# Kernel tuning notes

Hardware: AMD Instinct MI355X
Metric: run time of the kernel (lower is better)

## Reference

```python
import jax, jax.numpy as jnp
import numpy as np

B, L = 8, 2048
AMP, ANG = 48, 16
H = 4
AQK, GQK = 12, 6   # amp/ang qk head dims
AV, GV = 12, 6     # amp/ang v head dims
LOOKBACK = 100


def setup_inputs() -> dict:
    key = jax.random.key(0)
    ks = jax.random.split(key, 16)
    def w(k, i, o):
        # kaiming-uniform-ish scale; stored [in, out] so forward is x @ W
        bound = 1.0 / np.sqrt(i)
        return jax.random.uniform(k, (i, o), jnp.float32, -bound, bound)
    return dict(
        x_ang=jax.random.normal(ks[0], (B, L, 2 * ANG), jnp.float32),
        x_amp=jax.random.normal(ks[1], (B, L, AMP), jnp.float32),
        Wq_amp=w(ks[2], AMP, H * AQK),
        Wk_amp=w(ks[3], AMP, H * AQK),
        Wv_amp=w(ks[4], AMP, H * AV),
        Wq_ang_r=w(ks[5], ANG, H * GQK),
        Wq_ang_i=w(ks[6], ANG, H * GQK),
        Wk_ang_r=w(ks[7], ANG, H * GQK),
        Wk_ang_i=w(ks[8], ANG, H * GQK),
        Wv_ang_r=w(ks[9], ANG, H * GV),
        Wv_ang_i=w(ks[10], ANG, H * GV),
        Wout_amp=w(ks[11], H * AV, AMP),
        bout_amp=jax.random.uniform(ks[12], (AMP,), jnp.float32, -0.1, 0.1),
        Wout_ang_r=w(ks[13], H * GV, ANG),
        Wout_ang_i=w(ks[14], H * GV, ANG),
    )


def _clin(xr, xi, Wr, Wi):
    # complex linear: (xr + i xi) @ (Wr + i Wi)
    return xr @ Wr - xi @ Wi, xr @ Wi + xi @ Wr


def reference(x_ang, x_amp, Wq_amp, Wk_amp, Wv_amp,
              Wq_ang_r, Wq_ang_i, Wk_ang_r, Wk_ang_i,
              Wv_ang_r, Wv_ang_i, Wout_amp, bout_amp,
              Wout_ang_r, Wout_ang_i):
    Bb, Ll, CA = x_ang.shape
    ang_r, ang_i = jnp.split(x_ang, 2, axis=-1)

    def heads(x, hd):  # [B,L,H*hd] -> [B,H,L,hd]
        return x.reshape(Bb, Ll, H, hd).transpose(0, 2, 1, 3)

    q_amp = heads(x_amp @ Wq_amp, AQK)
    k_amp = heads(x_amp @ Wk_amp, AQK)
    qar, qai = _clin(ang_r, ang_i, Wq_ang_r, Wq_ang_i)
    kar, kai = _clin(ang_r, ang_i, Wk_ang_r, Wk_ang_i)
    q = jnp.concatenate([heads(qar, GQK), heads(qai, GQK), q_amp], axis=-1)  # [B,H,L,24]
    k = jnp.concatenate([heads(kar, GQK), heads(kai, GQK), k_amp], axis=-1)

    v_amp = heads(x_amp @ Wv_amp, AV)
    var, vai = _clin(ang_r, ang_i, Wv_ang_r, Wv_ang_i)
    v = jnp.concatenate([heads(var, GV), heads(vai, GV), v_amp], axis=-1)  # [B,H,L,24]

    scale = 1.0 / jnp.sqrt(jnp.asarray(q.shape[-1], q.dtype))
    scores = jnp.einsum('bhqd,bhkd->bhqk', q, k) * scale
    idx = jnp.arange(Ll)
    valid = (idx[None, :] <= idx[:, None]) & (idx[None, :] >= idx[:, None] - (LOOKBACK - 1))
    mask = jnp.where(valid, jnp.asarray(0.0, scores.dtype), jnp.finfo(scores.dtype).min)
    attn = jax.nn.softmax(scores + mask, axis=-1)
    out = jnp.einsum('bhqk,bhkd->bhqd', attn, v)  # [B,H,L,24]

    o_ang_r, o_ang_i, o_amp = jnp.split(out, [GV, 2 * GV], axis=-1)

    def merge(x):  # [B,H,L,hd] -> [B,L,H*hd]
        return x.transpose(0, 2, 1, 3).reshape(Bb, Ll, -1)

    out_amp = merge(o_amp) @ Wout_amp + bout_amp
    out_ang_r, out_ang_i = _clin(merge(o_ang_r), merge(o_ang_i), Wout_ang_r, Wout_ang_i)
    return (out_ang_r, out_ang_i, out_amp)
```

## Files before the change

kernel.cpp:

```cpp
#include <hip/hip_runtime.h>
#include <hip/hip_fp16.h>

constexpr int B = 8;
constexpr int L = 2048;
constexpr int ANG = 16;
constexpr int AMP = 48;
constexpr int H = 4;
constexpr int AQK = 12, GQK = 6;
constexpr int LOOKBACK = 100;
constexpr int NTOK = B * L;

typedef __fp16 f16x2 __attribute__((ext_vector_type(2)));

__device__ inline f16x2 pkrtz(float a, float b) {
    return __builtin_amdgcn_cvt_pkrtz(a, b);
}
__device__ inline float2 up2(f16x2 v) { return make_float2((float)v[0], (float)v[1]); }

__device__ inline float fdot2f(f16x2 a, f16x2 b, float c) {
#if __has_builtin(__builtin_amdgcn_fdot2)
    return __builtin_amdgcn_fdot2(a, b, c, false);
#else
    return c + (float)a[0] * (float)b[0] + (float)a[1] * (float)b[1];
#endif
}

union F4H { float4 v; f16x2 h[4]; };

constexpr int QT = 64;
constexpr int QKV_BLOCKS = NTOK / QT;

__global__ __launch_bounds__(256) void qkv6_kernel(
    const float* __restrict__ x_ang, const float* __restrict__ x_amp,
    const float* __restrict__ Wq_amp, const float* __restrict__ Wk_amp,
    const float* __restrict__ Wv_amp,
    const float* __restrict__ Wq_ang_r, const float* __restrict__ Wq_ang_i,
    const float* __restrict__ Wk_ang_r, const float* __restrict__ Wk_ang_i,
    const float* __restrict__ Wv_ang_r, const float* __restrict__ Wv_ang_i,
    __fp16* __restrict__ qg, __fp16* __restrict__ kg, __fp16* __restrict__ vg)
{
    __shared__ float xs[QT][81];
    const int tid  = threadIdx.x;
    const int tok0 = blockIdx.x * QT;

    {
        const float4* xm4 = (const float4*)(x_amp + (size_t)tok0 * AMP);
        for (int c = tid; c < QT * 12; c += 256) {
            int r = c / 12, i = c % 12;
            float4 t = xm4[c];
            float* p = &xs[r][4 * i];
            p[0]=t.x; p[1]=t.y; p[2]=t.z; p[3]=t.w;
        }
        const float4* xg4 = (const float4*)(x_ang + (size_t)tok0 * (2 * ANG));
        for (int c = tid; c < QT * 8; c += 256) {
            int r = c / 8, i = c % 8;
            float4 t = xg4[c];
            float* p = &xs[r][48 + 4 * i];
            p[0]=t.x; p[1]=t.y; p[2]=t.z; p[3]=t.w;
        }
    }
    __syncthreads();

    const int h  = tid >> 6;
    const int tl = tid & 63;

    float qd[24], kd[24], vd[24];
    #pragma unroll
    for (int c = 0; c < 24; ++c) { qd[c]=0.f; kd[c]=0.f; vd[c]=0.f; }

    #pragma unroll
    for (int i = 0; i < AMP; ++i) {
        float x = xs[tl][i];
        const float* wq = Wq_amp + i * 48 + h * AQK;
        const float* wk = Wk_amp + i * 48 + h * AQK;
        const float* wv = Wv_amp + i * 48 + h * AQK;
        #pragma unroll
        for (int c = 0; c < 12; ++c) {
            qd[12+c] += x * wq[c];
            kd[12+c] += x * wk[c];
            vd[12+c] += x * wv[c];
        }
    }
    #pragma unroll
    for (int i = 0; i < ANG; ++i) {
        float xr = xs[tl][48 + i], xi = xs[tl][64 + i];
        const float* wqr = Wq_ang_r + i * 24 + h * GQK;
        const float* wqi = Wq_ang_i + i * 24 + h * GQK;
        const float* wkr = Wk_ang_r + i * 24 + h * GQK;
        const float* wki = Wk_ang_i + i * 24 + h * GQK;
        const float* wvr = Wv_ang_r + i * 24 + h * GQK;
        const float* wvi = Wv_ang_i + i * 24 + h * GQK;
        #pragma unroll
        for (int c = 0; c < 6; ++c) {
            qd[c]   += xr * wqr[c] - xi * wqi[c];
            qd[6+c] += xr * wqi[c] + xi * wqr[c];
            kd[c]   += xr * wkr[c] - xi * wki[c];
            kd[6+c] += xr * wki[c] + xi * wkr[c];
            vd[c]   += xr * wvr[c] - xi * wvi[c];
            vd[6+c] += xr * wvi[c] + xi * wvr[c];
        }
    }

    const int bb = tok0 / L;
    const int ll = (tok0 % L) + tl;
    const size_t row = ((size_t)(bb * H + h) * L + ll) * 3;
    #pragma unroll
    for (int sl = 0; sl < 3; ++sl) {
        F4H fq, fk, fv;
        #pragma unroll
        for (int j = 0; j < 4; ++j) {
            fq.h[j] = pkrtz(qd[8*sl + 2*j], qd[8*sl + 2*j + 1]);
            fk.h[j] = pkrtz(kd[8*sl + 2*j], kd[8*sl + 2*j + 1]);
            fv.h[j] = pkrtz(vd[8*sl + 2*j], vd[8*sl + 2*j + 1]);
        }
        ((float4*)qg)[row + sl] = fq.v;
        ((float4*)kg)[row + sl] = fk.v;
        ((float4*)vg)[row + sl] = fv.v;
    }
}

constexpr int TQ     = 64;
constexpr int GROUPS = 4;
constexpr int CHUNK  = 25;
constexpr int MAXK   = TQ + LOOKBACK - 1;
constexpr int NT     = L / TQ;

__global__ __launch_bounds__(256, 2) void attn7_kernel(
    const __fp16* __restrict__ qg, const __fp16* __restrict__ kg,
    const __fp16* __restrict__ vg, float* __restrict__ att)
{
    __shared__ float4 Ks[MAXK][3];
    __shared__ float4 Vs[MAXK][3];

    const int tid = threadIdx.x;
    const int bh  = blockIdx.x / NT;
    const int qt  = blockIdx.x % NT;
    const int b   = bh / H, h = bh % H;
    const int q0  = qt * TQ;
    int kmin = q0 - (LOOKBACK - 1); if (kmin < 0) kmin = 0;
    const int nrows = q0 + TQ - kmin;

    {
        const float4* kb = (const float4*)kg + ((size_t)bh * L + kmin) * 3;
        const float4* vb = (const float4*)vg + ((size_t)bh * L + kmin) * 3;
        int ntot = nrows * 3;
        for (int c = tid; c < ntot; c += 256) {
            Ks[c / 3][c % 3] = kb[c];
            Vs[c / 3][c % 3] = vb[c];
        }
        float4 z = make_float4(0.f, 0.f, 0.f, 0.f);
        for (int c = ntot + tid; c < MAXK * 3; c += 256) {
            Ks[c / 3][c % 3] = z;
            Vs[c / 3][c % 3] = z;
        }
    }
    __syncthreads();

    const int lane = tid & 63;
    const int w    = tid >> 6;
    const int q16  = lane & 15;
    const int g    = lane >> 4;
    const int ql   = w * 16 + q16;
    const int qi   = q0 + ql;

    f16x2 qh[12];
    {
        const float4* qrow = (const float4*)qg + ((size_t)bh * L + qi) * 3;
        F4H a0, a1, a2;
        a0.v = qrow[0]; a1.v = qrow[1]; a2.v = qrow[2];
        #pragma unroll
        for (int j = 0; j < 4; ++j) {
            qh[j] = a0.h[j]; qh[4 + j] = a1.h[j]; qh[8 + j] = a2.h[j];
        }
    }

    const float scale = 0.2041241452319315f;
    int j0 = qi - (LOOKBACK - 1); if (j0 < 0) j0 = 0;
    const int jstart = j0 + g;

    float sc[CHUNK];
    #pragma unroll
    for (int t = 0; t < CHUNK; ++t) {
        int j = jstart + t * GROUPS;
        int r = j - kmin;
        F4H k0, k1, k2;
        k0.v = Ks[r][0]; k1.v = Ks[r][1]; k2.v = Ks[r][2];
        float d = 0.f;
        #pragma unroll
        for (int jj = 0; jj < 4; ++jj) d = fdot2f(qh[jj],     k0.h[jj], d);
        #pragma unroll
        for (int jj = 0; jj < 4; ++jj) d = fdot2f(qh[4 + jj], k1.h[jj], d);
        #pragma unroll
        for (int jj = 0; jj < 4; ++jj) d = fdot2f(qh[8 + jj], k2.h[jj], d);
        sc[t] = (j <= qi) ? d * scale : -3.0e38f;
    }
    float m = sc[0];
    #pragma unroll
    for (int t = 1; t < CHUNK; ++t) m = fmaxf(m, sc[t]);
    float ssum = 0.f;
    #pragma unroll
    for (int t = 0; t < CHUNK; ++t) {
        float p = __expf(sc[t] - m);
        p = (sc[t] > -1.0e37f) ? p : 0.f;
        sc[t] = p;
        ssum += p;
    }
    float o[24];
    #pragma unroll
    for (int e = 0; e < 24; ++e) o[e] = 0.f;
    #pragma unroll
    for (int t = 0; t < CHUNK; ++t) {
        float p = sc[t];
        int j = jstart + t * GROUPS;
        int r = j - kmin;
        #pragma unroll
        for (int sl = 0; sl < 3; ++sl) {
            F4H vv; vv.v = Vs[r][sl];
            #pragma unroll
            for (int jj = 0; jj < 4; ++jj) {
                float2 a = up2(vv.h[jj]);
                o[8*sl + 2*jj]     += p * a.x;
                o[8*sl + 2*jj + 1] += p * a.y;
            }
        }
    }

    #pragma unroll
    for (int d = 16; d <= 32; d <<= 1) {
        float m2 = __shfl_xor(m, d);
        float s2 = __shfl_xor(ssum, d);
        float mm = fmaxf(m, m2);
        float c1 = __expf(m - mm);
        float c2 = __expf(m2 - mm);
        ssum = ssum * c1 + s2 * c2;
        #pragma unroll
        for (int e = 0; e < 24; ++e)
            o[e] = o[e] * c1 + __shfl_xor(o[e], d) * c2;
        m = mm;
    }
    float inv = 1.f / ssum;

    {
        float4* dst = (float4*)att + (size_t)(b * L + qi) * 24 + h * 6;
        if (g == 0) {
            dst[0] = make_float4(o[0]*inv,  o[1]*inv,  o[2]*inv,  o[3]*inv);
            dst[4] = make_float4(o[16]*inv, o[17]*inv, o[18]*inv, o[19]*inv);
        } else if (g == 1) {
            dst[1] = make_float4(o[4]*inv,  o[5]*inv,  o[6]*inv,  o[7]*inv);
            dst[5] = make_float4(o[20]*inv, o[21]*inv, o[22]*inv, o[23]*inv);
        } else if (g == 2) {
            dst[2] = make_float4(o[8]*inv,  o[9]*inv,  o[10]*inv, o[11]*inv);
        } else {
            dst[3] = make_float4(o[12]*inv, o[13]*inv, o[14]*inv, o[15]*inv);
        }
    }
}

constexpr int PJ_AMP_BLOCKS = (NTOK * 12) / 256;
constexpr int PJ_ANG_BLOCKS = (NTOK * 4) / 256;

__global__ __launch_bounds__(256) void proj4_kernel(
    const float* __restrict__ att,
    const float* __restrict__ Wout_amp, const float* __restrict__ bout_amp,
    const float* __restrict__ Wout_ang_r, const float* __restrict__ Wout_ang_i,
    float* __restrict__ out)
{
    constexpr size_t ANG_OUT = (size_t)NTOK * ANG;
    int bid = blockIdx.x;

    if (bid < PJ_AMP_BLOCKS) {
        int gidx = bid * 256 + threadIdx.x;
        int c4   = (gidx % 12) * 4;
        int tok  = gidx / 12;
        const float4* at4 = (const float4*)att + (size_t)tok * 24;

        float a[48];
        #pragma unroll
        for (int h = 0; h < H; ++h) {
            #pragma unroll
            for (int i = 0; i < 3; ++i) {
                float4 t = at4[h * 6 + 3 + i];
                a[h*12 + 4*i+0]=t.x; a[h*12 + 4*i+1]=t.y;
                a[h*12 + 4*i+2]=t.z; a[h*12 + 4*i+3]=t.w;
            }
        }
        float4 acc = *(const float4*)(bout_amp + c4);
        #pragma unroll
        for (int i = 0; i < 48; ++i) {
            float4 w = *(const float4*)(Wout_amp + i * 48 + c4);
            acc.x += a[i]*w.x; acc.y += a[i]*w.y; acc.z += a[i]*w.z; acc.w += a[i]*w.w;
        }
        *(float4*)(out + 2*ANG_OUT + (size_t)tok * 48 + c4) = acc;
    } else {
        int gidx = (bid - PJ_AMP_BLOCKS) * 256 + threadIdx.x;
        int c4   = (gidx % 4) * 4;
        int tok  = gidx / 4;
        const float4* at4 = (const float4*)att + (size_t)tok * 24;

        float ar[24], ai[24];
        #pragma unroll
        for (int h = 0; h < H; ++h) {
            float4 t0 = at4[h*6+0], t1 = at4[h*6+1], t2 = at4[h*6+2];
            ar[h*6+0]=t0.x; ar[h*6+1]=t0.y; ar[h*6+2]=t0.z; ar[h*6+3]=t0.w;
            ar[h*6+4]=t1.x; ar[h*6+5]=t1.y;
            ai[h*6+0]=t1.z; ai[h*6+1]=t1.w;
            ai[h*6+2]=t2.x; ai[h*6+3]=t2.y; ai[h*6+4]=t2.z; ai[h*6+5]=t2.w;
        }
        float4 accr = make_float4(0.f,0.f,0.f,0.f);
        float4 acci = make_float4(0.f,0.f,0.f,0.f);
        #pragma unroll
        for (int i = 0; i < 24; ++i) {
            float4 wr = *(const float4*)(Wout_ang_r + i * 16 + c4);
            float4 wi = *(const float4*)(Wout_ang_i + i * 16 + c4);
            float r = ar[i], im = ai[i];
            accr.x += r*wr.x - im*wi.x;  accr.y += r*wr.y - im*wi.y;
            accr.z += r*wr.z - im*wi.z;  accr.w += r*wr.w - im*wi.w;
            acci.x += r*wi.x + im*wr.x;  acci.y += r*wi.y + im*wr.y;
            acci.z += r*wi.z + im*wr.z;  acci.w += r*wi.w + im*wr.w;
        }
        *(float4*)(out + (size_t)tok * 16 + c4)           = accr;
        *(float4*)(out + ANG_OUT + (size_t)tok * 16 + c4) = acci;
    }
}

extern "C" void kernel_launch(void* const* d_in, const int* in_sizes, int n_in,
                              void* d_out, int out_size, void* d_ws, size_t ws_size,
                              hipStream_t stream)
{
    const float* x_ang      = (const float*)d_in[0];
    const float* x_amp      = (const float*)d_in[1];
    const float* Wq_amp     = (const float*)d_in[2];
    const float* Wk_amp     = (const float*)d_in[3];
    const float* Wv_amp     = (const float*)d_in[4];
    const float* Wq_ang_r   = (const float*)d_in[5];
    const float* Wq_ang_i   = (const float*)d_in[6];
    const float* Wk_ang_r   = (const float*)d_in[7];
    const float* Wk_ang_i   = (const float*)d_in[8];
    const float* Wv_ang_r   = (const float*)d_in[9];
    const float* Wv_ang_i   = (const float*)d_in[10];
    const float* Wout_amp   = (const float*)d_in[11];
    const float* bout_amp   = (const float*)d_in[12];
    const float* Wout_ang_r = (const float*)d_in[13];
    const float* Wout_ang_i = (const float*)d_in[14];

    float* out = (float*)d_out;

    const size_t NQKV = (size_t)NTOK * H * 24;
    __fp16* qg = (__fp16*)d_ws;
    __fp16* kg = qg + NQKV;
    __fp16* vg = kg + NQKV;
    float*  att = (float*)(vg + NQKV);

    qkv6_kernel<<<QKV_BLOCKS, 256, 0, stream>>>(
        x_ang, x_amp, Wq_amp, Wk_amp, Wv_amp,
        Wq_ang_r, Wq_ang_i, Wk_ang_r, Wk_ang_i, Wv_ang_r, Wv_ang_i,
        qg, kg, vg);

    attn7_kernel<<<B * H * NT, 256, 0, stream>>>(qg, kg, vg, att);

    proj4_kernel<<<PJ_AMP_BLOCKS + PJ_ANG_BLOCKS, 256, 0, stream>>>(
        att, Wout_amp, bout_amp, Wout_ang_r, Wout_ang_i, out);
}
```

Before: 140.5 us.

## Fuse output projection into attention kernel via shared-memory staging across heads

Merges the attention kernel and the output-projection kernel into one. Each 512-thread block now handles all four heads for a 32-query tile and keeps the attention outputs in shared memory. It then applies the amp and complex ang projections directly from there. This removes the fp32 intermediate round-trip through global memory and one kernel launch. In exchange the block is larger, the query tile is smaller (so more K/V halo is reloaded per query), and the projection uses scalar weight loads.

```diff
diff --git a/kernel.cpp b/kernel.cpp
--- a/kernel.cpp
+++ b/kernel.cpp
@@ -119,58 +119,60 @@
     }
 }
 
-constexpr int TQ     = 64;
+constexpr int TQ2    = 32;
 constexpr int GROUPS = 4;
 constexpr int CHUNK  = 25;
-constexpr int MAXK   = TQ + LOOKBACK - 1;
-constexpr int NT     = L / TQ;
-
-__global__ __launch_bounds__(256, 2) void attn7_kernel(
+constexpr int MAXK2  = TQ2 + LOOKBACK - 1;
+constexpr int NT2    = L / TQ2;
+
+__global__ __launch_bounds__(512, 2) void attn_proj_kernel(
     const __fp16* __restrict__ qg, const __fp16* __restrict__ kg,
-    const __fp16* __restrict__ vg, float* __restrict__ att)
+    const __fp16* __restrict__ vg,
+    const float* __restrict__ Wout_amp, const float* __restrict__ bout_amp,
+    const float* __restrict__ Wout_ang_r, const float* __restrict__ Wout_ang_i,
+    float* __restrict__ out)
 {
-    __shared__ float4 Ks[MAXK][3];
-    __shared__ float4 Vs[MAXK][3];
+    __shared__ float4 Ks[H][MAXK2][3];
+    __shared__ float4 Vs[H][MAXK2][3];
+    __shared__ float  att_s[TQ2][100];
 
     const int tid = threadIdx.x;
-    const int bh  = blockIdx.x / NT;
-    const int qt  = blockIdx.x % NT;
-    const int b   = bh / H, h = bh % H;
-    const int q0  = qt * TQ;
+    const int b   = blockIdx.x >> 6;
+    const int qt  = blockIdx.x & 63;
+    const int q0  = qt * TQ2;
     int kmin = q0 - (LOOKBACK - 1); if (kmin < 0) kmin = 0;
-    const int nrows = q0 + TQ - kmin;
-
-    {
-        const float4* kb = (const float4*)kg + ((size_t)bh * L + kmin) * 3;
-        const float4* vb = (const float4*)vg + ((size_t)bh * L + kmin) * 3;
-        int ntot = nrows * 3;
-        for (int c = tid; c < ntot; c += 256) {
-            Ks[c / 3][c % 3] = kb[c];
-            Vs[c / 3][c % 3] = vb[c];
-        }
-        float4 z = make_float4(0.f, 0.f, 0.f, 0.f);
-        for (int c = ntot + tid; c < MAXK * 3; c += 256) {
-            Ks[c / 3][c % 3] = z;
-            Vs[c / 3][c % 3] = z;
+
+    {
+        const float4* kb = (const float4*)kg;
+        const float4* vb = (const float4*)vg;
+        for (int c = tid; c < H * MAXK2 * 3; c += 512) {
+            int hh  = c / (MAXK2 * 3);
+            int rem = c % (MAXK2 * 3);
+            int r   = rem / 3, sl = rem % 3;
+            size_t gi = ((size_t)(b * H + hh) * L + kmin + r) * 3 + sl;
+            Ks[hh][r][sl] = kb[gi];
+            Vs[hh][r][sl] = vb[gi];
         }
     }
     __syncthreads();
 
+    const int ww   = tid >> 6;
     const int lane = tid & 63;
-    const int w    = tid >> 6;
+    const int h    = ww & 3;
+    const int qh   = ww >> 2;
     const int q16  = lane & 15;
     const int g    = lane >> 4;
-    const int ql   = w * 16 + q16;
+    const int ql   = qh * 16 + q16;
     const int qi   = q0 + ql;
 
-    f16x2 qh[12];
-    {
-        const float4* qrow = (const float4*)qg + ((size_t)bh * L + qi) * 3;
+    f16x2 qhv[12];
+    {
+        const float4* qrow = (const float4*)qg + ((size_t)(b * H + h) * L + qi) * 3;
         F4H a0, a1, a2;
         a0.v = qrow[0]; a1.v = qrow[1]; a2.v = qrow[2];
         #pragma unroll
         for (int j = 0; j < 4; ++j) {
-            qh[j] = a0.h[j]; qh[4 + j] = a1.h[j]; qh[8 + j] = a2.h[j];
+            qhv[j] = a0.h[j]; qhv[4 + j] = a1.h[j]; qhv[8 + j] = a2.h[j];
         }
     }
 
@@ -184,14 +186,14 @@
         int j = jstart + t * GROUPS;
         int r = j - kmin;
         F4H k0, k1, k2;
-        k0.v = Ks[r][0]; k1.v = Ks[r][1]; k2.v = Ks[r][2];
+        k0.v = Ks[h][r][0]; k1.v = Ks[h][r][1]; k2.v = Ks[h][r][2];
         float d = 0.f;
         #pragma unroll
-        for (int jj = 0; jj < 4; ++jj) d = fdot2f(qh[jj],     k0.h[jj], d);
-        #pragma unroll
-        for (int jj = 0; jj < 4; ++jj) d = fdot2f(qh[4 + jj], k1.h[jj], d);
-        #pragma unroll
-        for (int jj = 0; jj < 4; ++jj) d = fdot2f(qh[8 + jj], k2.h[jj], d);
+        for (int jj = 0; jj < 4; ++jj) d = fdot2f(qhv[jj],     k0.h[jj], d);
+        #pragma unroll
+        for (int jj = 0; jj < 4; ++jj) d = fdot2f(qhv[4 + jj], k1.h[jj], d);
+        #pragma unroll
+        for (int jj = 0; jj < 4; ++jj) d = fdot2f(qhv[8 + jj], k2.h[jj], d);
         sc[t] = (j <= qi) ? d * scale : -3.0e38f;
     }
     float m = sc[0];
@@ -215,7 +217,7 @@
         int r = j - kmin;
         #pragma unroll
         for (int sl = 0; sl < 3; ++sl) {
-            F4H vv; vv.v = Vs[r][sl];
+            F4H vv; vv.v = Vs[h][r][sl];
             #pragma unroll
             for (int jj = 0; jj < 4; ++jj) {
                 float2 a = up2(vv.h[jj]);
@@ -241,85 +243,60 @@
     float inv = 1.f / ssum;
 
     {
-        float4* dst = (float4*)att + (size_t)(b * L + qi) * 24 + h * 6;
+        float* arow = &att_s[ql][h * 24];
         if (g == 0) {
-            dst[0] = make_float4(o[0]*inv,  o[1]*inv,  o[2]*inv,  o[3]*inv);
-            dst[4] = make_float4(o[16]*inv, o[17]*inv, o[18]*inv, o[19]*inv);
+            *(float4*)(arow +  0) = make_float4(o[0]*inv,  o[1]*inv,  o[2]*inv,  o[3]*inv);
+            *(float4*)(arow + 16) = make_float4(o[16]*inv, o[17]*inv, o[18]*inv, o[19]*inv);
         } else if (g == 1) {
-            dst[1] = make_float4(o[4]*inv,  o[5]*inv,  o[6]*inv,  o[7]*inv);
-            dst[5] = make_float4(o[20]*inv, o[21]*inv, o[22]*inv, o[23]*inv);
+            *(float4*)(arow +  4) = make_float4(o[4]*inv,  o[5]*inv,  o[6]*inv,  o[7]*inv);
+            *(float4*)(arow + 20) = make_float4(o[20]*inv, o[21]*inv, o[22]*inv, o[23]*inv);
         } else if (g == 2) {
-            dst[2] = make_float4(o[8]*inv,  o[9]*inv,  o[10]*inv, o[11]*inv);
+            *(float4*)(arow +  8) = make_float4(o[8]*inv,  o[9]*inv,  o[10]*inv, o[11]*inv);
         } else {
-            dst[3] = make_float4(o[12]*inv, o[13]*inv, o[14]*inv, o[15]*inv);
-        }
-    }
-}
-
-constexpr int PJ_AMP_BLOCKS = (NTOK * 12) / 256;
-constexpr int PJ_ANG_BLOCKS = (NTOK * 4) / 256;
-
-__global__ __launch_bounds__(256) void proj4_kernel(
-    const float* __restrict__ att,
-    const float* __restrict__ Wout_amp, const float* __restrict__ bout_amp,
-    const float* __restrict__ Wout_ang_r, const float* __restrict__ Wout_ang_i,
-    float* __restrict__ out)
-{
-    constexpr size_t ANG_OUT = (size_t)NTOK * ANG;
-    int bid = blockIdx.x;
-
-    if (bid < PJ_AMP_BLOCKS) {
-        int gidx = bid * 256 + threadIdx.x;
-        int c4   = (gidx % 12) * 4;
-        int tok  = gidx / 12;
-        const float4* at4 = (const float4*)att + (size_t)tok * 24;
-
-        float a[48];
-        #pragma unroll
-        for (int h = 0; h < H; ++h) {
+            *(float4*)(arow + 12) = make_float4(o[12]*inv, o[13]*inv, o[14]*inv, o[15]*inv);
+        }
+    }
+    __syncthreads();
+
+    {
+        constexpr size_t ANG_OUT = (size_t)NTOK * ANG;
+        const int tok = tid >> 4;
+        const int s   = tid & 15;
+        const float* arow = att_s[tok];
+        const size_t tokg = (size_t)b * L + q0 + tok;
+
+        float accr = 0.f, acci = 0.f;
+        #pragma unroll
+        for (int h2 = 0; h2 < H; ++h2) {
             #pragma unroll
-            for (int i = 0; i < 3; ++i) {
-                float4 t = at4[h * 6 + 3 + i];
-                a[h*12 + 4*i+0]=t.x; a[h*12 + 4*i+1]=t.y;
-                a[h*12 + 4*i+2]=t.z; a[h*12 + 4*i+3]=t.w;
+            for (int c = 0; c < 6; ++c) {
+                float ar = arow[h2*24 + c], ai = arow[h2*24 + 6 + c];
+                int rw = h2 * 6 + c;
+                float wr = Wout_ang_r[rw * 16 + s];
+                float wi = Wout_ang_i[rw * 16 + s];
+                accr += ar * wr - ai * wi;
+                acci += ar * wi + ai * wr;
             }
         }
-        float4 acc = *(const float4*)(bout_amp + c4);
-        #pragma unroll
-        for (int i = 0; i < 48; ++i) {
-            float4 w = *(const float4*)(Wout_amp + i * 48 + c4);
-            acc.x += a[i]*w.x; acc.y += a[i]*w.y; acc.z += a[i]*w.z; acc.w += a[i]*w.w;
-        }
-        *(float4*)(out + 2*ANG_OUT + (size_t)tok * 48 + c4) = acc;
-    } else {
-        int gidx = (bid - PJ_AMP_BLOCKS) * 256 + threadIdx.x;
-        int c4   = (gidx % 4) * 4;
-        int tok  = gidx / 4;
-        const float4* at4 = (const float4*)att + (size_t)tok * 24;
-
-        float ar[24], ai[24];
-        #pragma unroll
-        for (int h = 0; h < H; ++h) {
-            float4 t0 = at4[h*6+0], t1 = at4[h*6+1], t2 = at4[h*6+2];
-            ar[h*6+0]=t0.x; ar[h*6+1]=t0.y; ar[h*6+2]=t0.z; ar[h*6+3]=t0.w;
-            ar[h*6+4]=t1.x; ar[h*6+5]=t1.y;
-            ai[h*6+0]=t1.z; ai[h*6+1]=t1.w;
-            ai[h*6+2]=t2.x; ai[h*6+3]=t2.y; ai[h*6+4]=t2.z; ai[h*6+5]=t2.w;
-        }
-        float4 accr = make_float4(0.f,0.f,0.f,0.f);
-        float4 acci = make_float4(0.f,0.f,0.f,0.f);
-        #pragma unroll
-        for (int i = 0; i < 24; ++i) {
-            float4 wr = *(const float4*)(Wout_ang_r + i * 16 + c4);
-            float4 wi = *(const float4*)(Wout_ang_i + i * 16 + c4);
-            float r = ar[i], im = ai[i];
-            accr.x += r*wr.x - im*wi.x;  accr.y += r*wr.y - im*wi.y;
-            accr.z += r*wr.z - im*wi.z;  accr.w += r*wr.w - im*wi.w;
-            acci.x += r*wi.x + im*wr.x;  acci.y += r*wi.y + im*wr.y;
-            acci.z += r*wi.z + im*wr.z;  acci.w += r*wi.w + im*wr.w;
-        }
-        *(float4*)(out + (size_t)tok * 16 + c4)           = accr;
-        *(float4*)(out + ANG_OUT + (size_t)tok * 16 + c4) = acci;
+        out[tokg * 16 + s]           = accr;
+        out[ANG_OUT + tokg * 16 + s] = acci;
+
+        float a0 = bout_amp[s], a1 = bout_amp[s + 16], a2 = bout_amp[s + 32];
+        #pragma unroll
+        for (int h2 = 0; h2 < H; ++h2) {
+            #pragma unroll
+            for (int c = 0; c < 12; ++c) {
+                float xa = arow[h2*24 + 12 + c];
+                const float* wrow = Wout_amp + (h2 * 12 + c) * 48;
+                a0 += xa * wrow[s];
+                a1 += xa * wrow[s + 16];
+                a2 += xa * wrow[s + 32];
+            }
+        }
+        float* ob = out + 2 * ANG_OUT + tokg * 48;
+        ob[s]      = a0;
+        ob[s + 16] = a1;
+        ob[s + 32] = a2;
     }
 }
 
@@ -349,15 +326,12 @@
     __fp16* qg = (__fp16*)d_ws;
     __fp16* kg = qg + NQKV;
     __fp16* vg = kg + NQKV;
-    float*  att = (float*)(vg + NQKV);
 
     qkv6_kernel<<<QKV_BLOCKS, 256, 0, stream>>>(
         x_ang, x_amp, Wq_amp, Wk_amp, Wv_amp,
         Wq_ang_r, Wq_ang_i, Wk_ang_r, Wk_ang_i, Wv_ang_r, Wv_ang_i,
         qg, kg, vg);
 
-    attn7_kernel<<<B * H * NT, 256, 0, stream>>>(qg, kg, vg, att);
-
-    proj4_kernel<<<PJ_AMP_BLOCKS + PJ_ANG_BLOCKS, 256, 0, stream>>>(
-        att, Wout_amp, bout_amp, Wout_ang_r, Wout_ang_i, out);
-}
+    attn_proj_kernel<<<B * NT2, 512, 0, stream>>>(
+        qg, kg, vg, Wout_amp, bout_amp, Wout_ang_r, Wout_ang_i, out);
+}
```

New measurement: 137.0 us, median of 2. 2.5% less time.
